# Performance work log

Hardware: AMD Instinct MI355X
Metric: run time of the kernel (lower is better)

Reference implementation:

```python
import jax, jax.numpy as jnp
import numpy as np

D_MODEL = 1024
NUM_HEADS = 16
HEAD_DIM = D_MODEL // NUM_HEADS
B, S = 2, 2048


def setup_inputs() -> dict:
    key = jax.random.key(0)
    ks = jax.random.split(key, 12)
    sc = 1.0 / np.sqrt(D_MODEL)
    return {
        "x": jax.random.normal(ks[0], (B, S, D_MODEL), dtype=jnp.float32),
        "Wq": jax.random.normal(ks[1], (D_MODEL, D_MODEL), dtype=jnp.float32) * sc,
        "bq": jnp.zeros((D_MODEL,), dtype=jnp.float32),
        "Wk": jax.random.normal(ks[2], (D_MODEL, D_MODEL), dtype=jnp.float32) * sc,
        "bk": jnp.zeros((D_MODEL,), dtype=jnp.float32),
        "Wv": jax.random.normal(ks[3], (D_MODEL, D_MODEL), dtype=jnp.float32) * sc,
        "bv": jnp.zeros((D_MODEL,), dtype=jnp.float32),
        "Wo": jax.random.normal(ks[4], (D_MODEL, D_MODEL), dtype=jnp.float32) * sc,
        "bo": jnp.zeros((D_MODEL,), dtype=jnp.float32),
        "gate": jax.random.normal(ks[5], (NUM_HEADS, HEAD_DIM), dtype=jnp.float32),
        "ent": jax.random.normal(ks[6], (NUM_HEADS, HEAD_DIM, HEAD_DIM), dtype=jnp.float32)
            * (1.0 / np.sqrt(HEAD_DIM)),
    }


def reference(x, Wq, bq, Wk, bk, Wv, bv, Wo, bo, gate, ent):
    b, s, _ = x.shape
    # QKV projections (torch Linear: x @ W^T + b)
    q = (x @ Wq.T + bq).reshape(b, s, NUM_HEADS, HEAD_DIM).transpose(0, 2, 1, 3)  # bhsd
    k = (x @ Wk.T + bk).reshape(b, s, NUM_HEADS, HEAD_DIM).transpose(0, 2, 1, 3)
    v = (x @ Wv.T + bv).reshape(b, s, NUM_HEADS, HEAD_DIM).transpose(0, 2, 1, 3)
    # superposition gate: per-head, per-dim sigmoid gate broadcast over sequence
    q = q * jax.nn.sigmoid(gate)[None, :, None, :]
    # entanglement: per-head small matmul on keys
    k = jnp.einsum("bhsd,hde->bhse", k, ent)
    scores = jnp.einsum("bhqd,bhkd->bhqk", q, k) / np.sqrt(HEAD_DIM)
    attn = jax.nn.softmax(scores, axis=-1)
    ctx = jnp.einsum("bhqk,bhkd->bhqd", attn, v)
    ctx = ctx.transpose(0, 2, 1, 3).reshape(b, s, D_MODEL)
    out = ctx @ Wo.T + bo
    return (out, attn)
```

## Files before the change

### kernel.cpp

```cpp
#include <hip/hip_runtime.h>
#include <hip/hip_bf16.h>

#define DM 1024
#define NH 16
#define HD 64
#define BATCH 2
#define SEQ 2048
#define MROWS (BATCH*SEQ)

typedef __attribute__((ext_vector_type(8))) short bf16x8;
typedef __attribute__((ext_vector_type(4))) short bf16x4;
typedef __attribute__((ext_vector_type(4))) float f32x4;
typedef __attribute__((ext_vector_type(4))) unsigned u32x4;

#define LOG2E 1.44269504088896f

__device__ __forceinline__ short f2b(float f) {
  union { float f; unsigned u; } x; x.f = f;
  unsigned r = x.u + 0x7fffu + ((x.u >> 16) & 1u);
  return (short)(r >> 16);
}

__device__ __forceinline__ unsigned cvtpk(float lo, float hi) {
  unsigned r;
  asm("v_cvt_pk_bf16_f32 %0, %1, %2" : "=v"(r) : "v"(lo), "v"(hi));
  return r;
}

__device__ __forceinline__ float nexp2(float x) {
  return __builtin_amdgcn_exp2f(x);
}

__device__ __forceinline__ void lds_barrier() {
  asm volatile("s_waitcnt lgkmcnt(0)" ::: "memory");
  __builtin_amdgcn_s_barrier();
}

__device__ __forceinline__ void gload16(const void* g, void* l) {
  __builtin_amdgcn_global_load_lds((const __attribute__((address_space(1))) unsigned int*)g,
                                   (__attribute__((address_space(3))) unsigned int*)l, 16, 0, 0);
}

__global__ __launch_bounds__(256) void k_prep(
    const float* __restrict__ x,  const float* __restrict__ Wq,
    const float* __restrict__ Wk, const float* __restrict__ Wv,
    const float* __restrict__ Wo, const float* __restrict__ bq,
    const float* __restrict__ bk, const float* __restrict__ bv,
    const float* __restrict__ gate, const float* __restrict__ ent,
    short* __restrict__ xb, short* __restrict__ Wcat,
    short* __restrict__ Wob, float* __restrict__ bcat) {
  __shared__ float entL[4096];
  const int bid = blockIdx.x, t = threadIdx.x;
  if (bid < 2048) {
    int i = (bid * 256 + t) * 8;
    const float4* s4 = (const float4*)(x + i);
    float4 a = s4[0], b = s4[1];
    bf16x8 o;
    o[0]=f2b(a.x); o[1]=f2b(a.y); o[2]=f2b(a.z); o[3]=f2b(a.w);
    o[4]=f2b(b.x); o[5]=f2b(b.y); o[6]=f2b(b.z); o[7]=f2b(b.w);
    *(bf16x8*)(xb + i) = o;
  } else if (bid < 2560) {
    int i = ((bid - 2048) * 256 + t) * 8;
    int row = i >> 10;
    float sg = (0.125f * LOG2E) / (1.f + __expf(-gate[row]));
    const float4* s4 = (const float4*)(Wq + i);
    float4 a = s4[0], b = s4[1];
    bf16x8 o;
    o[0]=f2b(a.x*sg); o[1]=f2b(a.y*sg); o[2]=f2b(a.z*sg); o[3]=f2b(a.w*sg);
    o[4]=f2b(b.x*sg); o[5]=f2b(b.y*sg); o[6]=f2b(b.z*sg); o[7]=f2b(b.w*sg);
    *(bf16x8*)(Wcat + i) = o;
  } else if (bid < 2624) {
    int q = bid - 2560;
    int h = q >> 2, cc = q & 3;
    int c = cc * 256 + t;
#pragma unroll
    for (int j = 0; j < 16; ++j) entL[t + j*256] = ent[h*4096 + t + j*256];
    __syncthreads();
#pragma unroll 1
    for (int ec = 0; ec < 4; ++ec) {
      float acc[16];
#pragma unroll
      for (int e = 0; e < 16; ++e) acc[e] = 0.f;
#pragma unroll 4
      for (int d = 0; d < 64; ++d) {
        float wk = Wk[(size_t)(h*64 + d)*DM + c];
#pragma unroll
        for (int e = 0; e < 16; ++e) acc[e] += entL[d*64 + ec*16 + e] * wk;
      }
#pragma unroll
      for (int e = 0; e < 16; ++e)
        Wcat[(size_t)(1024 + h*64 + ec*16 + e)*DM + c] = f2b(acc[e]);
    }
  } else if (bid < 3136) {
    int i = ((bid - 2624) * 256 + t) * 8;
    const float4* s4 = (const float4*)(Wv + i);
    float4 a = s4[0], b = s4[1];
    bf16x8 o;
    o[0]=f2b(a.x); o[1]=f2b(a.y); o[2]=f2b(a.z); o[3]=f2b(a.w);
    o[4]=f2b(b.x); o[5]=f2b(b.y); o[6]=f2b(b.z); o[7]=f2b(b.w);
    *(bf16x8*)(Wcat + (size_t)2048*DM + i) = o;
  } else if (bid < 3648) {
    int i = ((bid - 3136) * 256 + t) * 8;
    const float4* s4 = (const float4*)(Wo + i);
    float4 a = s4[0], b = s4[1];
    bf16x8 o;
    o[0]=f2b(a.x); o[1]=f2b(a.y); o[2]=f2b(a.z); o[3]=f2b(a.w);
    o[4]=f2b(b.x); o[5]=f2b(b.y); o[6]=f2b(b.z); o[7]=f2b(b.w);
    *(bf16x8*)(Wob + i) = o;
  } else {
    int i = (bid - 3648) * 256 + t;
    float v;
    if (i < 1024) {
      v = bq[i] * ((0.125f * LOG2E) / (1.f + __expf(-gate[i])));
    } else if (i < 2048) {
      int rr = i - 1024, h = rr >> 6, e = rr & 63;
      float a = 0.f;
      for (int d = 0; d < 64; ++d) a += bk[h*64 + d] * ent[h*4096 + d*64 + e];
      v = a;
    } else {
      v = bv[i - 2048];
    }
    bcat[i] = v;
  }
}


template<int MODE, int LGX>
__global__ __launch_bounds__(256) void gemm_bt(const short* __restrict__ A,
                                               const short* __restrict__ B,
                                               const float* __restrict__ bias,
                                               void* __restrict__ C,
                                               short* __restrict__ vt,
                                               int M, int N, int K) {
  __shared__ __align__(16) short As[128*64];
  __shared__ __align__(16) short Bs[128*64];
  const int t = threadIdx.x, l = t & 63, w = t >> 6;
  const int wr = w >> 1, wc = w & 1;
  const int lin = blockIdx.x + (blockIdx.y << LGX);
  const int nwg = gridDim.x * gridDim.y;
  const int virt = (lin & 7) * (nwg >> 3) + (lin >> 3);
  const int bm = virt & ((1 << LGX) - 1), bn = virt >> LGX;
  const int row_l = l & 15, kg = l >> 4;
  f32x4 acc[4][4];
  {
    f32x4 z = {0.f, 0.f, 0.f, 0.f};
#pragma unroll
    for (int m = 0; m < 4; ++m)
#pragma unroll
      for (int n = 0; n < 4; ++n) acc[m][n] = z;
  }
  for (int k0 = 0; k0 < K; k0 += 64) {
#pragma unroll
    for (int i = 0; i < 4; ++i) {
      int idx = i * 256 + t;
      int row = idx >> 3, cb = (idx & 7) * 8;
      gload16(A + (size_t)(bm*128 + row)*K + k0 + cb, &As[idx*8]);
      gload16(B + (size_t)(bn*128 + row)*K + k0 + cb, &Bs[idx*8]);
    }
    __syncthreads();
#pragma unroll
    for (int ks = 0; ks < 2; ++ks) {
      bf16x8 af[4], bfv[4];
#pragma unroll
      for (int m = 0; m < 4; ++m)
        af[m] = *(const bf16x8*)&As[(wr*64 + m*16 + row_l)*64 + ks*32 + kg*8];
#pragma unroll
      for (int n = 0; n < 4; ++n)
        bfv[n] = *(const bf16x8*)&Bs[(wc*64 + n*16 + row_l)*64 + ks*32 + kg*8];
#pragma unroll
      for (int m = 0; m < 4; ++m)
#pragma unroll
        for (int n = 0; n < 4; ++n)
          acc[m][n] = __builtin_amdgcn_mfma_f32_16x16x32_bf16(af[m], bfv[n], acc[m][n], 0, 0, 0);
    }
    __syncthreads();
  }
  const int r0 = bm*128 + wr*64, c0 = bn*128 + wc*64;
  if (MODE == 1 && c0 >= 2048) {
    const int bb = (bm*128) >> 11;
#pragma unroll
    for (int n = 0; n < 4; ++n) {
      int cv = c0 + n*16 + row_l - 2048;
      int hh = cv >> 6, dd = cv & 63;
      float bvs = bias[c0 + n*16 + row_l];
      short* vrow = vt + ((size_t)((bb*16 + hh)*64 + dd))*SEQ;
#pragma unroll
      for (int m = 0; m < 4; ++m) {
        int s0 = (r0 + m*16 + kg*4) & (SEQ-1);
        bf16x4 o;
        o[0]=f2b(acc[m][n][0]+bvs); o[1]=f2b(acc[m][n][1]+bvs);
        o[2]=f2b(acc[m][n][2]+bvs); o[3]=f2b(acc[m][n][3]+bvs);
        *(bf16x4*)&vrow[s0] = o;
      }
    }
  } else {
#pragma unroll
    for (int n = 0; n < 4; ++n) {
      int col = c0 + n*16 + row_l;
      float bvs = bias[col];
#pragma unroll
      for (int m = 0; m < 4; ++m) {
#pragma unroll
        for (int r = 0; r < 4; ++r) {
          int row = r0 + m*16 + kg*4 + r;
          float v = acc[m][n][r] + bvs;
          if (MODE == 1) ((short*)C)[(size_t)row*2048 + col] = f2b(v);
          else           ((float*)C)[(size_t)row*N + col] = v;
        }
      }
    }
  }
}

__global__ __launch_bounds__(256) void gemm_bt_small(const short* __restrict__ A,
                                                     const short* __restrict__ B,
                                                     const float* __restrict__ bias,
                                                     float* __restrict__ C,
                                                     int M, int N, int K) {
  __shared__ __align__(16) short As[64*64];
  __shared__ __align__(16) short Bs[128*64];
  const int t = threadIdx.x, l = t & 63, w = t >> 6;
  const int wr = w >> 1, wc = w & 1;
  const int lin = blockIdx.x + (blockIdx.y << 6);
  const int nwg = gridDim.x * gridDim.y;
  const int virt = (lin & 7) * (nwg >> 3) + (lin >> 3);
  const int bm = virt & 63, bn = virt >> 6;
  const int row_l = l & 15, kg = l >> 4;
  f32x4 acc[2][4];
  {
    f32x4 z = {0.f, 0.f, 0.f, 0.f};
#pragma unroll
    for (int m = 0; m < 2; ++m)
#pragma unroll
      for (int n = 0; n < 4; ++n) acc[m][n] = z;
  }
  for (int k0 = 0; k0 < K; k0 += 64) {
#pragma unroll
    for (int i = 0; i < 2; ++i) {
      int idx = i * 256 + t;
      int row = idx >> 3, cb = (idx & 7) * 8;
      gload16(A + (size_t)(bm*64 + row)*K + k0 + cb, &As[idx*8]);
    }
#pragma unroll
    for (int i = 0; i < 4; ++i) {
      int idx = i * 256 + t;
      int row = idx >> 3, cb = (idx & 7) * 8;
      gload16(B + (size_t)(bn*128 + row)*K + k0 + cb, &Bs[idx*8]);
    }
    __syncthreads();
#pragma unroll
    for (int ks = 0; ks < 2; ++ks) {
      bf16x8 af[2], bfv[4];
#pragma unroll
      for (int m = 0; m < 2; ++m)
        af[m] = *(const bf16x8*)&As[(wr*32 + m*16 + row_l)*64 + ks*32 + kg*8];
#pragma unroll
      for (int n = 0; n < 4; ++n)
        bfv[n] = *(const bf16x8*)&Bs[(wc*64 + n*16 + row_l)*64 + ks*32 + kg*8];
#pragma unroll
      for (int m = 0; m < 2; ++m)
#pragma unroll
        for (int n = 0; n < 4; ++n)
          acc[m][n] = __builtin_amdgcn_mfma_f32_16x16x32_bf16(af[m], bfv[n], acc[m][n], 0, 0, 0);
    }
    __syncthreads();
  }
  const int r0 = bm*64 + wr*32, c0 = bn*128 + wc*64;
#pragma unroll
  for (int n = 0; n < 4; ++n) {
    int col = c0 + n*16 + row_l;
    float bvs = bias[col];
#pragma unroll
    for (int m = 0; m < 2; ++m) {
#pragma unroll
      for (int r = 0; r < 4; ++r) {
        int row = r0 + m*16 + kg*4 + r;
        C[(size_t)row*N + col] = acc[m][n][r] + bvs;
      }
    }
  }
}


__global__ __launch_bounds__(512) void attn_fused(const short* __restrict__ qk,
                                                  const short* __restrict__ vtg,
                                                  float* __restrict__ attn_out,
                                                  short* __restrict__ ctx) {
  __shared__ __align__(16) short Ks[2][64*64];
  __shared__ __align__(16) short Vt[2][64*64];
  const int t = threadIdx.x, l = t & 63, w = t >> 6;
  const int row_l = l & 15, kg = l >> 4;
  const int rsl = row_l & 7;
  const int blk = blockIdx.x;
  const int bh = blk >> 4, q0 = (blk & 15) * 128;
  const int b = bh >> 4, h = bh & 15;
  const short* Qp = qk + (size_t)b*SEQ*2048 + h*64;
  const short* Kp = qk + (size_t)b*SEQ*2048 + 1024 + h*64;
  const short* Vg = vtg + (size_t)bh*64*SEQ;
  float* attn_bh = attn_out + (size_t)bh*SEQ*SEQ;
  const int qw = q0 + w*16;

  const bf16x8 aq0 = *(const bf16x8*)(Qp + (size_t)(qw + row_l)*2048 + kg*8);
  const bf16x8 aq1 = *(const bf16x8*)(Qp + (size_t)(qw + row_l)*2048 + 32 + kg*8);

  const int a0 = t >> 3;
  const int c8 = (t & 7) * 8;
  const int g0 = (a0 & 0x23) | ((a0 & 0x0C) << 1) | ((a0 & 0x10) >> 2);
  const int wof0 = a0*64 + (c8 ^ ((a0 & 7) << 3));

  float rsum = 0.f;
  {
    bf16x8 rk0 = *(const bf16x8*)(Kp + (size_t)g0*2048 + c8);
    *(bf16x8*)&Ks[0][wof0] = rk0;
  }
  lds_barrier();
#pragma unroll 1
  for (int kt = 0; kt < 32; ++kt) {
    const int cur = kt & 1;
    bf16x8 rk0;
    if (kt < 31) {
      const short* kb = Kp + (size_t)(kt + 1)*64*2048;
      rk0 = *(const bf16x8*)(kb + (size_t)g0*2048 + c8);
    }
    __builtin_amdgcn_s_setprio(1);
#pragma unroll
    for (int nt = 0; nt < 4; ++nt) {
      const int row = nt*16 + row_l;
      bf16x8 k0 = *(const bf16x8*)&Ks[cur][row*64 + ((kg ^ rsl) << 3)];
      bf16x8 k1 = *(const bf16x8*)&Ks[cur][row*64 + (((kg|4) ^ rsl) << 3)];
      f32x4 s = {0.f, 0.f, 0.f, 0.f};
      s = __builtin_amdgcn_mfma_f32_16x16x32_bf16(k0, aq0, s, 0, 0, 0);
      s = __builtin_amdgcn_mfma_f32_16x16x32_bf16(k1, aq1, s, 0, 0, 0);
      rsum += (nexp2(s[0]) + nexp2(s[1])) + (nexp2(s[2]) + nexp2(s[3]));
    }
    __builtin_amdgcn_s_setprio(0);
    if (kt < 31) {
      *(bf16x8*)&Ks[cur^1][wof0] = rk0;
    }
    lds_barrier();
  }
  rsum += __shfl_xor(rsum, 16);
  rsum += __shfl_xor(rsum, 32);
  const float inv = 1.f / rsum;

  f32x4 actx[4];
  {
    f32x4 z = {0.f, 0.f, 0.f, 0.f};
#pragma unroll
    for (int e = 0; e < 4; ++e) actx[e] = z;
  }

  {
    bf16x8 rk0 = *(const bf16x8*)(Kp + (size_t)g0*2048 + c8);
    bf16x8 rv0 = *(const bf16x8*)(Vg + (size_t)a0*SEQ + c8);
    *(bf16x8*)&Ks[0][wof0] = rk0;
    *(bf16x8*)&Vt[0][wof0] = rv0;
  }
  lds_barrier();
#pragma unroll 1
  for (int kt = 0; kt < 32; ++kt) {
    const int cur = kt & 1;
    bf16x8 rk0, rv0;
    if (kt < 31) {
      const short* kb = Kp + (size_t)(kt + 1)*64*2048;
      const short* vb = Vg + (kt + 1)*64;
      rk0 = *(const bf16x8*)(kb + (size_t)g0*2048 + c8);
      rv0 = *(const bf16x8*)(vb + (size_t)a0*SEQ + c8);
    }
    f32x4 pf[4];
    __builtin_amdgcn_s_setprio(1);
#pragma unroll
    for (int nt = 0; nt < 4; ++nt) {
      const int row = nt*16 + row_l;
      bf16x8 k0 = *(const bf16x8*)&Ks[cur][row*64 + ((kg ^ rsl) << 3)];
      bf16x8 k1 = *(const bf16x8*)&Ks[cur][row*64 + (((kg|4) ^ rsl) << 3)];
      f32x4 s = {0.f, 0.f, 0.f, 0.f};
      s = __builtin_amdgcn_mfma_f32_16x16x32_bf16(k0, aq0, s, 0, 0, 0);
      s = __builtin_amdgcn_mfma_f32_16x16x32_bf16(k1, aq1, s, 0, 0, 0);
      f32x4 p;
      p[0] = nexp2(s[0]) * inv; p[1] = nexp2(s[1]) * inv;
      p[2] = nexp2(s[2]) * inv; p[3] = nexp2(s[3]) * inv;
      *(f32x4*)&attn_bh[(size_t)(qw + row_l)*SEQ + kt*64 + (nt&2)*16 + kg*8 + (nt&1)*4] = p;
      pf[nt] = p;
    }
#pragma unroll
    for (int hh = 0; hh < 2; ++hh) {
      u32x4 pq;
      pq[0] = cvtpk(pf[2*hh][0],   pf[2*hh][1]);
      pq[1] = cvtpk(pf[2*hh][2],   pf[2*hh][3]);
      pq[2] = cvtpk(pf[2*hh+1][0], pf[2*hh+1][1]);
      pq[3] = cvtpk(pf[2*hh+1][2], pf[2*hh+1][3]);
      bf16x8 pb = *(bf16x8*)&pq;
      const int vslot = ((kg | (hh << 2)) ^ rsl) << 3;
#pragma unroll
      for (int e = 0; e < 4; ++e) {
        bf16x8 va = *(const bf16x8*)&Vt[cur][(e*16 + row_l)*64 + vslot];
        actx[e] = __builtin_amdgcn_mfma_f32_16x16x32_bf16(va, pb, actx[e], 0, 0, 0);
      }
    }
    __builtin_amdgcn_s_setprio(0);
    if (kt < 31) {
      *(bf16x8*)&Ks[cur^1][wof0] = rk0;
      *(bf16x8*)&Vt[cur^1][wof0] = rv0;
    }
    lds_barrier();
  }
#pragma unroll
  for (int e = 0; e < 4; ++e) {
    int2 o;
    o.x = (int)cvtpk(actx[e][0], actx[e][1]);
    o.y = (int)cvtpk(actx[e][2], actx[e][3]);
    *(int2*)&ctx[(size_t)(b*SEQ + qw + row_l)*DM + h*64 + e*16 + kg*4] = o;
  }
}


extern "C" void kernel_launch(void* const* d_in, const int* in_sizes, int n_in,
                              void* d_out, int out_size, void* d_ws, size_t ws_size,
                              hipStream_t stream) {
  const float* x    = (const float*)d_in[0];
  const float* Wq   = (const float*)d_in[1];
  const float* bq   = (const float*)d_in[2];
  const float* Wk   = (const float*)d_in[3];
  const float* bk   = (const float*)d_in[4];
  const float* Wv   = (const float*)d_in[5];
  const float* bv   = (const float*)d_in[6];
  const float* Wo   = (const float*)d_in[7];
  const float* bo   = (const float*)d_in[8];
  const float* gate = (const float*)d_in[9];
  const float* ent  = (const float*)d_in[10];

  char* ws = (char*)d_ws;
  short* xb   = (short*)(ws);
  short* Wcat = (short*)(ws + ((size_t)8  << 20));
  short* Wob  = (short*)(ws + ((size_t)14 << 20));
  float* bcat = (float*)(ws + ((size_t)16 << 20));
  short* qkb  = (short*)(ws + ((size_t)17 << 20));
  short* vtg  = (short*)(ws + ((size_t)33 << 20));
  short* ctxb = xb;

  float* outp  = (float*)d_out;
  float* attnp = outp + (size_t)MROWS * DM;

  k_prep<<<3660, 256, 0, stream>>>(x, Wq, Wk, Wv, Wo, bq, bk, bv, gate, ent,
                                   xb, Wcat, Wob, bcat);
  gemm_bt<1, 5><<<dim3(32, 24), 256, 0, stream>>>(xb, Wcat, bcat, qkb, vtg, MROWS, 3072, DM);
  attn_fused<<<512, 512, 0, stream>>>(qkb, vtg, attnp, ctxb);
  gemm_bt_small<<<dim3(64, 8), 256, 0, stream>>>(ctxb, Wob, bo, outp, MROWS, DM, DM);
}
```

Baseline: 268.8 us.

## Drop LDS staging in attention; load K/V fragments directly from global

The attention kernel no longer stages K and V tiles through double-buffered shared memory with barriers. Each lane now loads its MFMA operand fragments straight from global memory, relying on L1/L2 caching for reuse across waves. Blocks shrink from 512 to 256 threads (64 query rows), and twice as many blocks are launched. This removes LDS writes and barrier stalls but adds redundant global and cache traffic, since every wave re-reads the same K/V rows.

Result: slower. 521.6 us (+94.1%).

```diff
diff --git a/kernel.cpp b/kernel.cpp
--- a/kernel.cpp
+++ b/kernel.cpp
@@ -29,11 +29,6 @@
 
 __device__ __forceinline__ float nexp2(float x) {
   return __builtin_amdgcn_exp2f(x);
-}
-
-__device__ __forceinline__ void lds_barrier() {
-  asm volatile("s_waitcnt lgkmcnt(0)" ::: "memory");
-  __builtin_amdgcn_s_barrier();
 }
 
 __device__ __forceinline__ void gload16(const void* g, void* l) {
@@ -282,17 +277,14 @@
 }
 
 
-__global__ __launch_bounds__(512) void attn_fused(const short* __restrict__ qk,
+__global__ __launch_bounds__(256) void attn_fused(const short* __restrict__ qk,
                                                   const short* __restrict__ vtg,
                                                   float* __restrict__ attn_out,
                                                   short* __restrict__ ctx) {
-  __shared__ __align__(16) short Ks[2][64*64];
-  __shared__ __align__(16) short Vt[2][64*64];
   const int t = threadIdx.x, l = t & 63, w = t >> 6;
   const int row_l = l & 15, kg = l >> 4;
-  const int rsl = row_l & 7;
   const int blk = blockIdx.x;
-  const int bh = blk >> 4, q0 = (blk & 15) * 128;
+  const int bh = blk >> 5, q0 = (blk & 31) * 64;
   const int b = bh >> 4, h = bh & 15;
   const short* Qp = qk + (size_t)b*SEQ*2048 + h*64;
   const short* Kp = qk + (size_t)b*SEQ*2048 + 1024 + h*64;
@@ -303,41 +295,24 @@
   const bf16x8 aq0 = *(const bf16x8*)(Qp + (size_t)(qw + row_l)*2048 + kg*8);
   const bf16x8 aq1 = *(const bf16x8*)(Qp + (size_t)(qw + row_l)*2048 + 32 + kg*8);
 
-  const int a0 = t >> 3;
-  const int c8 = (t & 7) * 8;
-  const int g0 = (a0 & 0x23) | ((a0 & 0x0C) << 1) | ((a0 & 0x10) >> 2);
-  const int wof0 = a0*64 + (c8 ^ ((a0 & 7) << 3));
+  const int kgrow = (row_l & 3) | ((row_l & 0xC) << 1);
+  const short* kb_lane = Kp + (size_t)kgrow*2048 + kg*8;
+  const short* vb_lane = Vg + (size_t)row_l*SEQ;
 
   float rsum = 0.f;
-  {
-    bf16x8 rk0 = *(const bf16x8*)(Kp + (size_t)g0*2048 + c8);
-    *(bf16x8*)&Ks[0][wof0] = rk0;
-  }
-  lds_barrier();
 #pragma unroll 1
   for (int kt = 0; kt < 32; ++kt) {
-    const int cur = kt & 1;
-    bf16x8 rk0;
-    if (kt < 31) {
-      const short* kb = Kp + (size_t)(kt + 1)*64*2048;
-      rk0 = *(const bf16x8*)(kb + (size_t)g0*2048 + c8);
-    }
-    __builtin_amdgcn_s_setprio(1);
+    const short* kb = kb_lane + (size_t)kt*64*2048;
 #pragma unroll
     for (int nt = 0; nt < 4; ++nt) {
-      const int row = nt*16 + row_l;
-      bf16x8 k0 = *(const bf16x8*)&Ks[cur][row*64 + ((kg ^ rsl) << 3)];
-      bf16x8 k1 = *(const bf16x8*)&Ks[cur][row*64 + (((kg|4) ^ rsl) << 3)];
+      const size_t off = (size_t)(((nt & 1) * 4 + (nt & 2) * 16)) * 2048;
+      bf16x8 k0 = *(const bf16x8*)(kb + off);
+      bf16x8 k1 = *(const bf16x8*)(kb + off + 32);
       f32x4 s = {0.f, 0.f, 0.f, 0.f};
       s = __builtin_amdgcn_mfma_f32_16x16x32_bf16(k0, aq0, s, 0, 0, 0);
       s = __builtin_amdgcn_mfma_f32_16x16x32_bf16(k1, aq1, s, 0, 0, 0);
       rsum += (nexp2(s[0]) + nexp2(s[1])) + (nexp2(s[2]) + nexp2(s[3]));
     }
-    __builtin_amdgcn_s_setprio(0);
-    if (kt < 31) {
-      *(bf16x8*)&Ks[cur^1][wof0] = rk0;
-    }
-    lds_barrier();
   }
   rsum += __shfl_xor(rsum, 16);
   rsum += __shfl_xor(rsum, 32);
@@ -350,30 +325,15 @@
     for (int e = 0; e < 4; ++e) actx[e] = z;
   }
 
-  {
-    bf16x8 rk0 = *(const bf16x8*)(Kp + (size_t)g0*2048 + c8);
-    bf16x8 rv0 = *(const bf16x8*)(Vg + (size_t)a0*SEQ + c8);
-    *(bf16x8*)&Ks[0][wof0] = rk0;
-    *(bf16x8*)&Vt[0][wof0] = rv0;
-  }
-  lds_barrier();
 #pragma unroll 1
   for (int kt = 0; kt < 32; ++kt) {
-    const int cur = kt & 1;
-    bf16x8 rk0, rv0;
-    if (kt < 31) {
-      const short* kb = Kp + (size_t)(kt + 1)*64*2048;
-      const short* vb = Vg + (kt + 1)*64;
-      rk0 = *(const bf16x8*)(kb + (size_t)g0*2048 + c8);
-      rv0 = *(const bf16x8*)(vb + (size_t)a0*SEQ + c8);
-    }
+    const short* kb = kb_lane + (size_t)kt*64*2048;
     f32x4 pf[4];
-    __builtin_amdgcn_s_setprio(1);
 #pragma unroll
     for (int nt = 0; nt < 4; ++nt) {
-      const int row = nt*16 + row_l;
-      bf16x8 k0 = *(const bf16x8*)&Ks[cur][row*64 + ((kg ^ rsl) << 3)];
-      bf16x8 k1 = *(const bf16x8*)&Ks[cur][row*64 + (((kg|4) ^ rsl) << 3)];
+      const size_t off = (size_t)(((nt & 1) * 4 + (nt & 2) * 16)) * 2048;
+      bf16x8 k0 = *(const bf16x8*)(kb + off);
+      bf16x8 k1 = *(const bf16x8*)(kb + off + 32);
       f32x4 s = {0.f, 0.f, 0.f, 0.f};
       s = __builtin_amdgcn_mfma_f32_16x16x32_bf16(k0, aq0, s, 0, 0, 0);
       s = __builtin_amdgcn_mfma_f32_16x16x32_bf16(k1, aq1, s, 0, 0, 0);
@@ -391,19 +351,13 @@
       pq[2] = cvtpk(pf[2*hh+1][0], pf[2*hh+1][1]);
       pq[3] = cvtpk(pf[2*hh+1][2], pf[2*hh+1][3]);
       bf16x8 pb = *(bf16x8*)&pq;
-      const int vslot = ((kg | (hh << 2)) ^ rsl) << 3;
+      const int vcol = kt*64 + hh*32 + kg*8;
 #pragma unroll
       for (int e = 0; e < 4; ++e) {
-        bf16x8 va = *(const bf16x8*)&Vt[cur][(e*16 + row_l)*64 + vslot];
+        bf16x8 va = *(const bf16x8*)(vb_lane + (size_t)e*16*SEQ + vcol);
         actx[e] = __builtin_amdgcn_mfma_f32_16x16x32_bf16(va, pb, actx[e], 0, 0, 0);
       }
     }
-    __builtin_amdgcn_s_setprio(0);
-    if (kt < 31) {
-      *(bf16x8*)&Ks[cur^1][wof0] = rk0;
-      *(bf16x8*)&Vt[cur^1][wof0] = rv0;
-    }
-    lds_barrier();
   }
 #pragma unroll
   for (int e = 0; e < 4; ++e) {
@@ -445,6 +399,6 @@
   k_prep<<<3660, 256, 0, stream>>>(x, Wq, Wk, Wv, Wo, bq, bk, bv, gate, ent,
                                    xb, Wcat, Wob, bcat);
   gemm_bt<1, 5><<<dim3(32, 24), 256, 0, stream>>>(xb, Wcat, bcat, qkb, vtg, MROWS, 3072, DM);
-  attn_fused<<<512, 512, 0, stream>>>(qkb, vtg, attnp, ctxb);
+  attn_fused<<<1024, 256, 0, stream>>>(qkb, vtg, attnp, ctxb);
   gemm_bt_small<<<dim3(64, 8), 256, 0, stream>>>(ctxb, Wob, bo, outp, MROWS, DM, DM);
 }
```
